# Kernel optimization log

Hardware: AMD Instinct MI355X
Metric: run time of the kernel (lower is better)

The kernel has to match this reference:

```python
import jax, jax.numpy as jnp
import numpy as np

NUM_ACTIVE = 2  # num_active from init


def setup_inputs() -> dict:
    key = jax.random.key(0)
    k1, k2, k3, k4 = jax.random.split(key, 4)
    B, S, D, H, E = 2, 1024, 1024, 4096, 8
    x = jax.random.normal(k1, (B, S, D), jnp.float32)
    # router initialized to zeros in the torch module, but we use small random
    # weights so routing is non-degenerate for the correctness baseline
    router_w = jax.random.normal(k2, (D, E), jnp.float32) * 0.02
    router_b = jnp.zeros((E,), jnp.float32)
    w12 = jax.random.normal(k3, (E, D, 2 * H), jnp.float32) * (1.0 / np.sqrt(D))
    w3 = jax.random.normal(k4, (E, H, D), jnp.float32) * (1.0 / np.sqrt(H))
    return {"x": x, "router_w": router_w, "router_b": router_b, "w12": w12, "w3": w3}


def reference(x, router_w, router_b, w12, w3):
    E = router_w.shape[-1]
    # router (eval mode: no jitter noise)
    logits = x @ router_w + router_b                      # [B,S,E]
    scores = jax.nn.sigmoid(logits)
    top_s, top_i = jax.lax.top_k(scores, NUM_ACTIVE)      # [B,S,k]
    rw = top_s / (jnp.sum(top_s, axis=-1, keepdims=True) + 1e-6)
    # per-token combine weight for each expert: sum of routed slot weights
    cw = jnp.sum(jax.nn.one_hot(top_i, E, dtype=x.dtype) * rw[..., None], axis=-2)  # [B,S,E]
    # dense all-expert SwiGLU (same math as masked loop in the original)
    x12 = jnp.einsum('bsd,edh->ebsh', x, w12)             # [E,B,S,2H]
    x1, x2 = jnp.split(x12, 2, axis=-1)
    h = jax.nn.silu(x1) * x2                              # [E,B,S,H]
    out = jnp.einsum('ebsh,ehd,bse->bsd', h, w3, cw)      # [B,S,D]
    aux_loss = 0.01 * jnp.mean(logits ** 2)
    return out, aux_loss
```

## Files before the change

### kernel.cpp

```cpp
#include <hip/hip_runtime.h>
#include <hip/hip_bf16.h>

#define TOK 2048
#define DIM 1024
#define HID 4096
#define NE  8

typedef short bf16x8 __attribute__((ext_vector_type(8)));
typedef float f32x4 __attribute__((ext_vector_type(4)));
typedef unsigned short ushort_t;
typedef unsigned int uint_t;

#define SWZB(n) (((((n) >> 2) ^ ((n) >> 4)) & 3) << 4)

__device__ __forceinline__ ushort_t f2bf(float f) {
  uint_t b = __float_as_uint(f);
  uint_t r = (b + 0x7FFFu + ((b >> 16) & 1u)) >> 16;
  return (ushort_t)r;
}
__device__ __forceinline__ float bf2f(ushort_t u) {
  return __uint_as_float(((uint_t)u) << 16);
}
__device__ __forceinline__ uint_t pk2bf(float a, float b) {
  uint_t r;
  asm("v_cvt_pk_bf16_f32 %0, %1, %2" : "=v"(r) : "v"(a), "v"(b));
  return r;
}

__global__ void router_kernel(const float* __restrict__ x,
                              const float* __restrict__ rw,
                              const float* __restrict__ rb,
                              float* __restrict__ tok_ss,
                              int* __restrict__ top_e,
                              float* __restrict__ top_w,
                              ushort_t* __restrict__ xb) {
  const int t = blockIdx.x;
  const int lane = threadIdx.x;
  float acc[NE];
#pragma unroll
  for (int e = 0; e < NE; ++e) acc[e] = 0.f;
  const float4* x4 = (const float4*)(x + (size_t)t * DIM);
  uint2* xb2 = (uint2*)(xb + (size_t)t * DIM);
#pragma unroll
  for (int j = 0; j < 4; ++j) {
    int i = j * 64 + lane;
    float4 v = x4[i];
    uint2 u;
    u.x = pk2bf(v.x, v.y);
    u.y = pk2bf(v.z, v.w);
    xb2[i] = u;
    const float* w = rw + (size_t)i * 4 * NE;
    const float* vp = (const float*)&v;
#pragma unroll
    for (int c = 0; c < 4; ++c)
#pragma unroll
      for (int e = 0; e < NE; ++e) acc[e] += vp[c] * w[c * NE + e];
  }
#pragma unroll
  for (int e = 0; e < NE; ++e) {
    float v = acc[e];
#pragma unroll
    for (int off = 32; off > 0; off >>= 1) v += __shfl_down(v, off, 64);
    acc[e] = v;
  }
  if (lane == 0) {
    float sc[NE];
    float ss = 0.f;
#pragma unroll
    for (int e = 0; e < NE; ++e) {
      float lg = acc[e] + rb[e];
      ss += lg * lg;
      sc[e] = 1.f / (1.f + expf(-lg));
    }
    tok_ss[t] = ss;
    int i0 = 0;
#pragma unroll
    for (int e = 1; e < NE; ++e) if (sc[e] > sc[i0]) i0 = e;
    int i1 = (i0 == 0) ? 1 : 0;
#pragma unroll
    for (int e = 0; e < NE; ++e) if (e != i0 && sc[e] > sc[i1]) i1 = e;
    float s0 = sc[i0], s1 = sc[i1];
    float inv = 1.f / (s0 + s1 + 1e-6f);
    top_e[t * 2 + 0] = i0;
    top_e[t * 2 + 1] = i1;
    top_w[t * 2 + 0] = s0 * inv;
    top_w[t * 2 + 1] = s1 * inv;
  }
}

__global__ void scan_assign_kernel(const int* __restrict__ top_e,
                                   const float* __restrict__ top_w,
                                   int* __restrict__ offsets,
                                   int* __restrict__ list_tok,
                                   float* __restrict__ list_w,
                                   int* __restrict__ pair_pos) {
  __shared__ int lcount[NE];
  __shared__ int loff[NE + 1];
  __shared__ int lfill[NE];
  if (threadIdx.x < NE) lcount[threadIdx.x] = 0;
  __syncthreads();
  for (int i = threadIdx.x; i < TOK * 2; i += 256)
    atomicAdd(&lcount[top_e[i]], 1);
  __syncthreads();
  if (threadIdx.x == 0) {
    int o = 0;
    for (int e = 0; e < NE; ++e) { loff[e] = o; lfill[e] = o; o += lcount[e]; }
    loff[NE] = o;
  }
  __syncthreads();
  if (threadIdx.x <= NE) offsets[threadIdx.x] = loff[threadIdx.x];
  for (int i = threadIdx.x; i < TOK * 2; i += 256) {
    int e = top_e[i];
    int idx = atomicAdd(&lfill[e], 1);
    list_tok[idx] = i >> 1;
    list_w[idx] = top_w[i];
    pair_pos[i] = idx;
  }
}

__global__ void aux_kernel(const float* __restrict__ tok_ss, float* __restrict__ out_aux) {
  __shared__ float sm[256];
  float s = 0.f;
  for (int t = threadIdx.x; t < TOK; t += 256) s += tok_ss[t];
  sm[threadIdx.x] = s;
  __syncthreads();
  for (int w = 128; w > 0; w >>= 1) {
    if (threadIdx.x < w) sm[threadIdx.x] += sm[threadIdx.x + w];
    __syncthreads();
  }
  if (threadIdx.x == 0) *out_aux = 0.01f * sm[0] / (float)(TOK * NE);
}

__global__ __launch_bounds__(256)
void gemm1_mfma(const ushort_t* __restrict__ xb,
                const float* __restrict__ w12,
                const int* __restrict__ offsets, const int* __restrict__ list_tok,
                ushort_t* __restrict__ hhi) {
  __shared__ __align__(16) ushort_t Ah[128 * 40];
  __shared__ __align__(16) ushort_t B1[128 * 40];
  __shared__ __align__(16) ushort_t B2[128 * 40];
  __shared__ int stok[128];

  const int e = blockIdx.y >> 4;
  const int rt = blockIdx.y & 15;
  const int rowstart = offsets[e] + rt * 128;
  const int rowend = offsets[e + 1];
  if (rowstart >= rowend) return;
  const int h0 = blockIdx.x * 128;
  const int tid = threadIdx.x;
  const int lane = tid & 63, wid = tid >> 6;
  const int wm = wid >> 1, wn = wid & 1;
  const int lr = lane & 15, kh = lane >> 4;

  if (tid < 128) {
    int r = rowstart + tid;
    stok[tid] = list_tok[r < rowend ? r : rowstart];
  }
  __syncthreads();

  f32x4 acc1[4][4], acc2[4][4];
#pragma unroll
  for (int mi = 0; mi < 4; ++mi)
#pragma unroll
    for (int nj = 0; nj < 4; ++nj) {
      acc1[mi][nj] = (f32x4){0.f, 0.f, 0.f, 0.f};
      acc2[mi][nj] = (f32x4){0.f, 0.f, 0.f, 0.f};
    }

  const int arow0 = tid >> 2, aseg = tid & 3;
  const int arow1 = arow0 + 64;
  const size_t asrc0 = (size_t)stok[arow0] * DIM + aseg * 8;
  const size_t asrc1 = (size_t)stok[arow1] * DIM + aseg * 8;
  const int adst0 = arow0 * 40 + aseg * 8;
  const int adst1 = arow1 * 40 + aseg * 8;

  const int p = tid >> 4, n4 = tid & 15;
  const float* w12e = w12 + (size_t)e * DIM * (2 * HID) + h0 + n4 * 4;
  char* B1c = (char*)B1;
  char* B2c = (char*)B2;

  int boff[4];
#pragma unroll
  for (int nj = 0; nj < 4; ++nj) {
    int n = wn * 64 + nj * 16 + lr;
    boff[nj] = n * 80 + ((kh * 16) ^ SWZB(n));
  }
  int bwoff[4], bwoff2[4];
#pragma unroll
  for (int c = 0; c < 4; ++c) {
    int n = n4 * 4 + c;
    bwoff[c] = n * 80 + ((4 * p) ^ SWZB(n));
    int n2 = 64 + n;
    bwoff2[c] = n2 * 80 + ((4 * p) ^ SWZB(n2));
  }

  uint4 ra0, ra1;
  float4 w1a, w1b, w1c, w1d, w2a, w2b, w2c, w2d;
#define G1_LOAD(K0) do { \
    ra0 = *(const uint4*)&xb[asrc0 + (K0)]; \
    ra1 = *(const uint4*)&xb[asrc1 + (K0)]; \
    const float* r0 = w12e + (size_t)((K0) + 2 * p) * (2 * HID); \
    w1a = *(const float4*)r0; \
    w1b = *(const float4*)(r0 + 2 * HID); \
    w1c = *(const float4*)(r0 + 64); \
    w1d = *(const float4*)(r0 + 2 * HID + 64); \
    w2a = *(const float4*)(r0 + HID); \
    w2b = *(const float4*)(r0 + HID + 2 * HID); \
    w2c = *(const float4*)(r0 + HID + 64); \
    w2d = *(const float4*)(r0 + HID + 2 * HID + 64); \
  } while (0)

  G1_LOAD(0);
#pragma unroll 1
  for (int k0 = 0; k0 < DIM; k0 += 32) {
    *(uint4*)&Ah[adst0] = ra0;
    *(uint4*)&Ah[adst1] = ra1;
    {
      const float* p1a = (const float*)&w1a;
      const float* p1b = (const float*)&w1b;
      const float* p1c = (const float*)&w1c;
      const float* p1d = (const float*)&w1d;
      const float* p2a = (const float*)&w2a;
      const float* p2b = (const float*)&w2b;
      const float* p2c = (const float*)&w2c;
      const float* p2d = (const float*)&w2d;
#pragma unroll
      for (int c = 0; c < 4; ++c) {
        *(uint_t*)(B1c + bwoff[c])  = pk2bf(p1a[c], p1b[c]);
        *(uint_t*)(B2c + bwoff[c])  = pk2bf(p2a[c], p2b[c]);
        *(uint_t*)(B1c + bwoff2[c]) = pk2bf(p1c[c], p1d[c]);
        *(uint_t*)(B2c + bwoff2[c]) = pk2bf(p2c[c], p2d[c]);
      }
    }
    __syncthreads();
    if (k0 + 32 < DIM) G1_LOAD(k0 + 32);

    bf16x8 af[4], b1f[4], b2f[4];
#pragma unroll
    for (int mi = 0; mi < 4; ++mi)
      af[mi] = *(bf16x8*)&Ah[(wm * 64 + mi * 16 + lr) * 40 + kh * 8];
#pragma unroll
    for (int nj = 0; nj < 4; ++nj) {
      b1f[nj] = *(bf16x8*)(B1c + boff[nj]);
      b2f[nj] = *(bf16x8*)(B2c + boff[nj]);
    }
#pragma unroll
    for (int mi = 0; mi < 4; ++mi)
#pragma unroll
      for (int nj = 0; nj < 4; ++nj) {
        acc1[mi][nj] = __builtin_amdgcn_mfma_f32_16x16x32_bf16(af[mi], b1f[nj], acc1[mi][nj], 0, 0, 0);
        acc2[mi][nj] = __builtin_amdgcn_mfma_f32_16x16x32_bf16(af[mi], b2f[nj], acc2[mi][nj], 0, 0, 0);
      }
    __syncthreads();
  }
#undef G1_LOAD

#pragma unroll
  for (int mi = 0; mi < 4; ++mi)
#pragma unroll
    for (int nj = 0; nj < 4; ++nj)
#pragma unroll
      for (int r = 0; r < 4; ++r) {
        int row_t = wm * 64 + mi * 16 + kh * 4 + r;
        int gr = rowstart + row_t;
        if (gr < rowend) {
          int col = h0 + wn * 64 + nj * 16 + lr;
          float v1 = acc1[mi][nj][r], v2 = acc2[mi][nj][r];
          float hv = (v1 / (1.f + expf(-v1))) * v2;
          hhi[(size_t)gr * HID + col] = f2bf(hv);
        }
      }
}

__global__ __launch_bounds__(256)
void gemm2_mfma(const ushort_t* __restrict__ hhi,
                const float* __restrict__ w3,
                const int* __restrict__ offsets, const float* __restrict__ list_w,
                ushort_t* __restrict__ pairout) {
  __shared__ __align__(16) ushort_t As0[64 * 40];
  __shared__ __align__(16) ushort_t As1[64 * 40];
  __shared__ __align__(16) ushort_t Bs0[64 * 40];
  __shared__ __align__(16) ushort_t Bs1[64 * 40];

  const int e = blockIdx.y >> 4;
  const int rt = blockIdx.y & 15;
  const int rowstart = offsets[e] + rt * 64;
  const int rowend = offsets[e + 1];
  if (rowstart >= rowend) return;
  const int d0 = blockIdx.x * 64;
  const int tid = threadIdx.x;
  const int lane = tid & 63, wid = tid >> 6;
  const int wm = wid >> 1, wn = wid & 1;
  const int lr = lane & 15, kh = lane >> 4;

  f32x4 acc[2][2];
#pragma unroll
  for (int mi = 0; mi < 2; ++mi)
#pragma unroll
    for (int nj = 0; nj < 2; ++nj) acc[mi][nj] = (f32x4){0.f, 0.f, 0.f, 0.f};

  const int arow = tid >> 2, aseg = tid & 3;
  int gr = rowstart + arow; if (gr >= rowend) gr = rowstart;
  const size_t asrc = (size_t)gr * HID + aseg * 8;
  const int adst = arow * 40 + aseg * 8;

  const int p = tid >> 4, n4 = tid & 15;
  const float* w3e = w3 + (size_t)e * HID * DIM + d0 + n4 * 4;
  char* Bs0c = (char*)Bs0;
  char* Bs1c = (char*)Bs1;

  int boff[2];
#pragma unroll
  for (int nj = 0; nj < 2; ++nj) {
    int n = wn * 32 + nj * 16 + lr;
    boff[nj] = n * 80 + ((kh * 16) ^ SWZB(n));
  }
  int bwoff[4];
#pragma unroll
  for (int c = 0; c < 4; ++c) {
    int n = n4 * 4 + c;
    bwoff[c] = n * 80 + ((4 * p) ^ SWZB(n));
  }

  uint4 ra0, ra1;
  float4 rb00, rb01, rb10, rb11;
#define G2_LOAD(K0) do { \
    ra0 = *(const uint4*)&hhi[asrc + (K0)]; \
    ra1 = *(const uint4*)&hhi[asrc + (K0) + 32]; \
    const float* r0 = w3e + (size_t)((K0) + 2 * p) * DIM; \
    rb00 = *(const float4*)r0; \
    rb01 = *(const float4*)(r0 + DIM); \
    const float* r1 = w3e + (size_t)((K0) + 32 + 2 * p) * DIM; \
    rb10 = *(const float4*)r1; \
    rb11 = *(const float4*)(r1 + DIM); \
  } while (0)

  const int NT = HID / 64;
  G2_LOAD(0);
#pragma unroll 1
  for (int k0 = 0; k0 < HID; k0 += 64) {
    *(uint4*)&As0[adst] = ra0;
    *(uint4*)&As1[adst] = ra1;
    {
      const float* pv0 = (const float*)&rb00;
      const float* pv1 = (const float*)&rb01;
      const float* pw0 = (const float*)&rb10;
      const float* pw1 = (const float*)&rb11;
#pragma unroll
      for (int c = 0; c < 4; ++c) {
        *(uint_t*)(Bs0c + bwoff[c]) = pk2bf(pv0[c], pv1[c]);
        *(uint_t*)(Bs1c + bwoff[c]) = pk2bf(pw0[c], pw1[c]);
      }
    }
    __syncthreads();
    if (k0 + 64 < HID) G2_LOAD(k0 + 64);

    {
      bf16x8 af[2], bf[2];
#pragma unroll
      for (int mi = 0; mi < 2; ++mi)
        af[mi] = *(bf16x8*)&As0[(wm * 32 + mi * 16 + lr) * 40 + kh * 8];
#pragma unroll
      for (int nj = 0; nj < 2; ++nj)
        bf[nj] = *(bf16x8*)(Bs0c + boff[nj]);
#pragma unroll
      for (int mi = 0; mi < 2; ++mi)
#pragma unroll
        for (int nj = 0; nj < 2; ++nj)
          acc[mi][nj] = __builtin_amdgcn_mfma_f32_16x16x32_bf16(af[mi], bf[nj], acc[mi][nj], 0, 0, 0);
    }
    {
      bf16x8 af[2], bf[2];
#pragma unroll
      for (int mi = 0; mi < 2; ++mi)
        af[mi] = *(bf16x8*)&As1[(wm * 32 + mi * 16 + lr) * 40 + kh * 8];
#pragma unroll
      for (int nj = 0; nj < 2; ++nj)
        bf[nj] = *(bf16x8*)(Bs1c + boff[nj]);
#pragma unroll
      for (int mi = 0; mi < 2; ++mi)
#pragma unroll
        for (int nj = 0; nj < 2; ++nj)
          acc[mi][nj] = __builtin_amdgcn_mfma_f32_16x16x32_bf16(af[mi], bf[nj], acc[mi][nj], 0, 0, 0);
    }
    __syncthreads();
  }
#undef G2_LOAD

#pragma unroll
  for (int mi = 0; mi < 2; ++mi)
#pragma unroll
    for (int nj = 0; nj < 2; ++nj)
#pragma unroll
      for (int r = 0; r < 4; ++r) {
        int grr = rowstart + wm * 32 + mi * 16 + kh * 4 + r;
        if (grr < rowend) {
          int col = d0 + wn * 32 + nj * 16 + lr;
          pairout[(size_t)grr * DIM + col] = f2bf(acc[mi][nj][r] * list_w[grr]);
        }
      }
}

__global__ void combine_bf(const ushort_t* __restrict__ pairout,
                           const int* __restrict__ pair_pos,
                           float* __restrict__ out) {
  int i = blockIdx.x * 256 + threadIdx.x;
  int t = i >> 8;
  int dv = i & 255;
  int p0 = pair_pos[2 * t], p1 = pair_pos[2 * t + 1];
  ushort4 a = *(const ushort4*)&pairout[(size_t)p0 * DIM + dv * 4];
  ushort4 b = *(const ushort4*)&pairout[(size_t)p1 * DIM + dv * 4];
  float4 o;
  o.x = bf2f(a.x) + bf2f(b.x);
  o.y = bf2f(a.y) + bf2f(b.y);
  o.z = bf2f(a.z) + bf2f(b.z);
  o.w = bf2f(a.w) + bf2f(b.w);
  ((float4*)out)[i] = o;
}

extern "C" void kernel_launch(void* const* d_in, const int* in_sizes, int n_in,
                              void* d_out, int out_size, void* d_ws, size_t ws_size,
                              hipStream_t stream) {
  const float* x   = (const float*)d_in[0];
  const float* rw  = (const float*)d_in[1];
  const float* rb  = (const float*)d_in[2];
  const float* w12 = (const float*)d_in[3];
  const float* w3  = (const float*)d_in[4];
  float* out = (float*)d_out;

  char* ws = (char*)d_ws;
  size_t off = 0;
  auto alloc = [&](size_t bytes) {
    void* p = ws + off;
    off = (off + bytes + 255) & ~255ULL;
    return p;
  };
  int*   offsets  = (int*)alloc((NE + 1) * 4);
  float* tok_ss   = (float*)alloc(TOK * 4);
  int*   top_e    = (int*)alloc(TOK * 2 * 4);
  float* top_w    = (float*)alloc(TOK * 2 * 4);
  int*   list_tok = (int*)alloc(TOK * 2 * 4);
  float* list_w   = (float*)alloc(TOK * 2 * 4);
  int*   pair_pos = (int*)alloc(TOK * 2 * 4);

  ushort_t* xb      = (ushort_t*)alloc((size_t)TOK * DIM * 2);
  ushort_t* hhi     = (ushort_t*)alloc((size_t)TOK * 2 * HID * 2);
  ushort_t* pairoutb= (ushort_t*)alloc((size_t)TOK * 2 * DIM * 2);

  hipLaunchKernelGGL(router_kernel, dim3(TOK), dim3(64), 0, stream,
                     x, rw, rb, tok_ss, top_e, top_w, xb);
  hipLaunchKernelGGL(scan_assign_kernel, dim3(1), dim3(256), 0, stream,
                     top_e, top_w, offsets, list_tok, list_w, pair_pos);
  hipLaunchKernelGGL(aux_kernel, dim3(1), dim3(256), 0, stream,
                     tok_ss, out + (size_t)TOK * DIM);

  hipLaunchKernelGGL(gemm1_mfma, dim3(HID / 128, NE * 16), dim3(256), 0, stream,
                     xb, w12, offsets, list_tok, hhi);
  hipLaunchKernelGGL(gemm2_mfma, dim3(DIM / 64, NE * 16), dim3(256), 0, stream,
                     hhi, w3, offsets, list_w, pairoutb);
  hipLaunchKernelGGL(combine_bf, dim3(TOK * DIM / 4 / 256), dim3(256), 0, stream,
                     pairoutb, pair_pos, out);
}
```

Before: 356.4 us.

## Fuse combine into gemm2 via atomics; narrow gemm1 tile with 64-wide K steps

Removes the separate combine kernel and the bf16 pairout buffer. gemm2 now scatters its weighted results straight into the fp32 output with atomicAdd, after a memset of the output. gemm1's N tile is halved to 64 columns, which doubles the grid, and each iteration now handles a K step of 64 in two 32-wide halves, so there are half as many barriers. The atomics add contention, the per-token sum order becomes nondeterministic, and gemm1 now re-reads the activations across twice as many column blocks.

```diff
diff --git a/kernel.cpp b/kernel.cpp
--- a/kernel.cpp
+++ b/kernel.cpp
@@ -92,8 +92,7 @@
                                    const float* __restrict__ top_w,
                                    int* __restrict__ offsets,
                                    int* __restrict__ list_tok,
-                                   float* __restrict__ list_w,
-                                   int* __restrict__ pair_pos) {
+                                   float* __restrict__ list_w) {
   __shared__ int lcount[NE];
   __shared__ int loff[NE + 1];
   __shared__ int lfill[NE];
@@ -114,7 +113,6 @@
     int idx = atomicAdd(&lfill[e], 1);
     list_tok[idx] = i >> 1;
     list_w[idx] = top_w[i];
-    pair_pos[i] = idx;
   }
 }
 
@@ -136,9 +134,12 @@
                 const float* __restrict__ w12,
                 const int* __restrict__ offsets, const int* __restrict__ list_tok,
                 ushort_t* __restrict__ hhi) {
-  __shared__ __align__(16) ushort_t Ah[128 * 40];
-  __shared__ __align__(16) ushort_t B1[128 * 40];
-  __shared__ __align__(16) ushort_t B2[128 * 40];
+  __shared__ __align__(16) ushort_t Ah0[128 * 40];
+  __shared__ __align__(16) ushort_t Ah1[128 * 40];
+  __shared__ __align__(16) ushort_t B1h0[64 * 40];
+  __shared__ __align__(16) ushort_t B1h1[64 * 40];
+  __shared__ __align__(16) ushort_t B2h0[64 * 40];
+  __shared__ __align__(16) ushort_t B2h1[64 * 40];
   __shared__ int stok[128];
 
   const int e = blockIdx.y >> 4;
@@ -146,7 +147,7 @@
   const int rowstart = offsets[e] + rt * 128;
   const int rowend = offsets[e + 1];
   if (rowstart >= rowend) return;
-  const int h0 = blockIdx.x * 128;
+  const int h0 = blockIdx.x * 64;
   const int tid = threadIdx.x;
   const int lane = tid & 63, wid = tid >> 6;
   const int wm = wid >> 1, wn = wid & 1;
@@ -158,11 +159,11 @@
   }
   __syncthreads();
 
-  f32x4 acc1[4][4], acc2[4][4];
+  f32x4 acc1[4][2], acc2[4][2];
 #pragma unroll
   for (int mi = 0; mi < 4; ++mi)
 #pragma unroll
-    for (int nj = 0; nj < 4; ++nj) {
+    for (int nj = 0; nj < 2; ++nj) {
       acc1[mi][nj] = (f32x4){0.f, 0.f, 0.f, 0.f};
       acc2[mi][nj] = (f32x4){0.f, 0.f, 0.f, 0.f};
     }
@@ -176,81 +177,106 @@
 
   const int p = tid >> 4, n4 = tid & 15;
   const float* w12e = w12 + (size_t)e * DIM * (2 * HID) + h0 + n4 * 4;
-  char* B1c = (char*)B1;
-  char* B2c = (char*)B2;
-
-  int boff[4];
-#pragma unroll
-  for (int nj = 0; nj < 4; ++nj) {
-    int n = wn * 64 + nj * 16 + lr;
+  char* B1c0 = (char*)B1h0;
+  char* B1c1 = (char*)B1h1;
+  char* B2c0 = (char*)B2h0;
+  char* B2c1 = (char*)B2h1;
+
+  int boff[2];
+#pragma unroll
+  for (int nj = 0; nj < 2; ++nj) {
+    int n = wn * 32 + nj * 16 + lr;
     boff[nj] = n * 80 + ((kh * 16) ^ SWZB(n));
   }
-  int bwoff[4], bwoff2[4];
+  int bwoff[4];
 #pragma unroll
   for (int c = 0; c < 4; ++c) {
     int n = n4 * 4 + c;
     bwoff[c] = n * 80 + ((4 * p) ^ SWZB(n));
-    int n2 = 64 + n;
-    bwoff2[c] = n2 * 80 + ((4 * p) ^ SWZB(n2));
-  }
-
-  uint4 ra0, ra1;
-  float4 w1a, w1b, w1c, w1d, w2a, w2b, w2c, w2d;
+  }
+
+  uint4 ra00, ra10, ra01, ra11;
+  float4 w1a0, w1b0, w2a0, w2b0, w1a1, w1b1, w2a1, w2b1;
 #define G1_LOAD(K0) do { \
-    ra0 = *(const uint4*)&xb[asrc0 + (K0)]; \
-    ra1 = *(const uint4*)&xb[asrc1 + (K0)]; \
+    ra00 = *(const uint4*)&xb[asrc0 + (K0)]; \
+    ra10 = *(const uint4*)&xb[asrc1 + (K0)]; \
+    ra01 = *(const uint4*)&xb[asrc0 + (K0) + 32]; \
+    ra11 = *(const uint4*)&xb[asrc1 + (K0) + 32]; \
     const float* r0 = w12e + (size_t)((K0) + 2 * p) * (2 * HID); \
-    w1a = *(const float4*)r0; \
-    w1b = *(const float4*)(r0 + 2 * HID); \
-    w1c = *(const float4*)(r0 + 64); \
-    w1d = *(const float4*)(r0 + 2 * HID + 64); \
-    w2a = *(const float4*)(r0 + HID); \
-    w2b = *(const float4*)(r0 + HID + 2 * HID); \
-    w2c = *(const float4*)(r0 + HID + 64); \
-    w2d = *(const float4*)(r0 + HID + 2 * HID + 64); \
+    w1a0 = *(const float4*)r0; \
+    w1b0 = *(const float4*)(r0 + 2 * HID); \
+    w2a0 = *(const float4*)(r0 + HID); \
+    w2b0 = *(const float4*)(r0 + HID + 2 * HID); \
+    const float* r1 = w12e + (size_t)((K0) + 32 + 2 * p) * (2 * HID); \
+    w1a1 = *(const float4*)r1; \
+    w1b1 = *(const float4*)(r1 + 2 * HID); \
+    w2a1 = *(const float4*)(r1 + HID); \
+    w2b1 = *(const float4*)(r1 + HID + 2 * HID); \
   } while (0)
 
   G1_LOAD(0);
 #pragma unroll 1
-  for (int k0 = 0; k0 < DIM; k0 += 32) {
-    *(uint4*)&Ah[adst0] = ra0;
-    *(uint4*)&Ah[adst1] = ra1;
-    {
-      const float* p1a = (const float*)&w1a;
-      const float* p1b = (const float*)&w1b;
-      const float* p1c = (const float*)&w1c;
-      const float* p1d = (const float*)&w1d;
-      const float* p2a = (const float*)&w2a;
-      const float* p2b = (const float*)&w2b;
-      const float* p2c = (const float*)&w2c;
-      const float* p2d = (const float*)&w2d;
+  for (int k0 = 0; k0 < DIM; k0 += 64) {
+    *(uint4*)&Ah0[adst0] = ra00;
+    *(uint4*)&Ah0[adst1] = ra10;
+    *(uint4*)&Ah1[adst0] = ra01;
+    *(uint4*)&Ah1[adst1] = ra11;
+    {
+      const float* p1a0 = (const float*)&w1a0;
+      const float* p1b0 = (const float*)&w1b0;
+      const float* p2a0 = (const float*)&w2a0;
+      const float* p2b0 = (const float*)&w2b0;
+      const float* p1a1 = (const float*)&w1a1;
+      const float* p1b1 = (const float*)&w1b1;
+      const float* p2a1 = (const float*)&w2a1;
+      const float* p2b1 = (const float*)&w2b1;
 #pragma unroll
       for (int c = 0; c < 4; ++c) {
-        *(uint_t*)(B1c + bwoff[c])  = pk2bf(p1a[c], p1b[c]);
-        *(uint_t*)(B2c + bwoff[c])  = pk2bf(p2a[c], p2b[c]);
-        *(uint_t*)(B1c + bwoff2[c]) = pk2bf(p1c[c], p1d[c]);
-        *(uint_t*)(B2c + bwoff2[c]) = pk2bf(p2c[c], p2d[c]);
+        *(uint_t*)(B1c0 + bwoff[c]) = pk2bf(p1a0[c], p1b0[c]);
+        *(uint_t*)(B2c0 + bwoff[c]) = pk2bf(p2a0[c], p2b0[c]);
+        *(uint_t*)(B1c1 + bwoff[c]) = pk2bf(p1a1[c], p1b1[c]);
+        *(uint_t*)(B2c1 + bwoff[c]) = pk2bf(p2a1[c], p2b1[c]);
       }
     }
     __syncthreads();
-    if (k0 + 32 < DIM) G1_LOAD(k0 + 32);
-
-    bf16x8 af[4], b1f[4], b2f[4];
-#pragma unroll
-    for (int mi = 0; mi < 4; ++mi)
-      af[mi] = *(bf16x8*)&Ah[(wm * 64 + mi * 16 + lr) * 40 + kh * 8];
-#pragma unroll
-    for (int nj = 0; nj < 4; ++nj) {
-      b1f[nj] = *(bf16x8*)(B1c + boff[nj]);
-      b2f[nj] = *(bf16x8*)(B2c + boff[nj]);
-    }
-#pragma unroll
-    for (int mi = 0; mi < 4; ++mi)
-#pragma unroll
-      for (int nj = 0; nj < 4; ++nj) {
-        acc1[mi][nj] = __builtin_amdgcn_mfma_f32_16x16x32_bf16(af[mi], b1f[nj], acc1[mi][nj], 0, 0, 0);
-        acc2[mi][nj] = __builtin_amdgcn_mfma_f32_16x16x32_bf16(af[mi], b2f[nj], acc2[mi][nj], 0, 0, 0);
-      }
+    if (k0 + 64 < DIM) G1_LOAD(k0 + 64);
+
+    {
+      bf16x8 af[4], b1f[2], b2f[2];
+#pragma unroll
+      for (int mi = 0; mi < 4; ++mi)
+        af[mi] = *(bf16x8*)&Ah0[(wm * 64 + mi * 16 + lr) * 40 + kh * 8];
+#pragma unroll
+      for (int nj = 0; nj < 2; ++nj) {
+        b1f[nj] = *(bf16x8*)(B1c0 + boff[nj]);
+        b2f[nj] = *(bf16x8*)(B2c0 + boff[nj]);
+      }
+#pragma unroll
+      for (int mi = 0; mi < 4; ++mi)
+#pragma unroll
+        for (int nj = 0; nj < 2; ++nj) {
+          acc1[mi][nj] = __builtin_amdgcn_mfma_f32_16x16x32_bf16(af[mi], b1f[nj], acc1[mi][nj], 0, 0, 0);
+          acc2[mi][nj] = __builtin_amdgcn_mfma_f32_16x16x32_bf16(af[mi], b2f[nj], acc2[mi][nj], 0, 0, 0);
+        }
+    }
+    {
+      bf16x8 af[4], b1f[2], b2f[2];
+#pragma unroll
+      for (int mi = 0; mi < 4; ++mi)
+        af[mi] = *(bf16x8*)&Ah1[(wm * 64 + mi * 16 + lr) * 40 + kh * 8];
+#pragma unroll
+      for (int nj = 0; nj < 2; ++nj) {
+        b1f[nj] = *(bf16x8*)(B1c1 + boff[nj]);
+        b2f[nj] = *(bf16x8*)(B2c1 + boff[nj]);
+      }
+#pragma unroll
+      for (int mi = 0; mi < 4; ++mi)
+#pragma unroll
+        for (int nj = 0; nj < 2; ++nj) {
+          acc1[mi][nj] = __builtin_amdgcn_mfma_f32_16x16x32_bf16(af[mi], b1f[nj], acc1[mi][nj], 0, 0, 0);
+          acc2[mi][nj] = __builtin_amdgcn_mfma_f32_16x16x32_bf16(af[mi], b2f[nj], acc2[mi][nj], 0, 0, 0);
+        }
+    }
     __syncthreads();
   }
 #undef G1_LOAD
@@ -258,13 +284,13 @@
 #pragma unroll
   for (int mi = 0; mi < 4; ++mi)
 #pragma unroll
-    for (int nj = 0; nj < 4; ++nj)
+    for (int nj = 0; nj < 2; ++nj)
 #pragma unroll
       for (int r = 0; r < 4; ++r) {
         int row_t = wm * 64 + mi * 16 + kh * 4 + r;
         int gr = rowstart + row_t;
         if (gr < rowend) {
-          int col = h0 + wn * 64 + nj * 16 + lr;
+          int col = h0 + wn * 32 + nj * 16 + lr;
           float v1 = acc1[mi][nj][r], v2 = acc2[mi][nj][r];
           float hv = (v1 / (1.f + expf(-v1))) * v2;
           hhi[(size_t)gr * HID + col] = f2bf(hv);
@@ -276,7 +302,8 @@
 void gemm2_mfma(const ushort_t* __restrict__ hhi,
                 const float* __restrict__ w3,
                 const int* __restrict__ offsets, const float* __restrict__ list_w,
-                ushort_t* __restrict__ pairout) {
+                const int* __restrict__ list_tok,
+                float* __restrict__ out) {
   __shared__ __align__(16) ushort_t As0[64 * 40];
   __shared__ __align__(16) ushort_t As1[64 * 40];
   __shared__ __align__(16) ushort_t Bs0[64 * 40];
@@ -335,7 +362,6 @@
     rb11 = *(const float4*)(r1 + DIM); \
   } while (0)
 
-  const int NT = HID / 64;
   G2_LOAD(0);
 #pragma unroll 1
   for (int k0 = 0; k0 < HID; k0 += 64) {
@@ -396,26 +422,10 @@
         int grr = rowstart + wm * 32 + mi * 16 + kh * 4 + r;
         if (grr < rowend) {
           int col = d0 + wn * 32 + nj * 16 + lr;
-          pairout[(size_t)grr * DIM + col] = f2bf(acc[mi][nj][r] * list_w[grr]);
+          int tok = list_tok[grr];
+          atomicAdd(&out[(size_t)tok * DIM + col], acc[mi][nj][r] * list_w[grr]);
         }
       }
-}
-
-__global__ void combine_bf(const ushort_t* __restrict__ pairout,
-                           const int* __restrict__ pair_pos,
-                           float* __restrict__ out) {
-  int i = blockIdx.x * 256 + threadIdx.x;
-  int t = i >> 8;
-  int dv = i & 255;
-  int p0 = pair_pos[2 * t], p1 = pair_pos[2 * t + 1];
-  ushort4 a = *(const ushort4*)&pairout[(size_t)p0 * DIM + dv * 4];
-  ushort4 b = *(const ushort4*)&pairout[(size_t)p1 * DIM + dv * 4];
-  float4 o;
-  o.x = bf2f(a.x) + bf2f(b.x);
-  o.y = bf2f(a.y) + bf2f(b.y);
-  o.z = bf2f(a.z) + bf2f(b.z);
-  o.w = bf2f(a.w) + bf2f(b.w);
-  ((float4*)out)[i] = o;
 }
 
 extern "C" void kernel_launch(void* const* d_in, const int* in_sizes, int n_in,
@@ -441,23 +451,21 @@
   float* top_w    = (float*)alloc(TOK * 2 * 4);
   int*   list_tok = (int*)alloc(TOK * 2 * 4);
   float* list_w   = (float*)alloc(TOK * 2 * 4);
-  int*   pair_pos = (int*)alloc(TOK * 2 * 4);
-
-  ushort_t* xb      = (ushort_t*)alloc((size_t)TOK * DIM * 2);
-  ushort_t* hhi     = (ushort_t*)alloc((size_t)TOK * 2 * HID * 2);
-  ushort_t* pairoutb= (ushort_t*)alloc((size_t)TOK * 2 * DIM * 2);
+
+  ushort_t* xb  = (ushort_t*)alloc((size_t)TOK * DIM * 2);
+  ushort_t* hhi = (ushort_t*)alloc((size_t)TOK * 2 * HID * 2);
+
+  hipMemsetAsync(out, 0, (size_t)TOK * DIM * 4, stream);
 
   hipLaunchKernelGGL(router_kernel, dim3(TOK), dim3(64), 0, stream,
                      x, rw, rb, tok_ss, top_e, top_w, xb);
   hipLaunchKernelGGL(scan_assign_kernel, dim3(1), dim3(256), 0, stream,
-                     top_e, top_w, offsets, list_tok, list_w, pair_pos);
+                     top_e, top_w, offsets, list_tok, list_w);
   hipLaunchKernelGGL(aux_kernel, dim3(1), dim3(256), 0, stream,
                      tok_ss, out + (size_t)TOK * DIM);
 
-  hipLaunchKernelGGL(gemm1_mfma, dim3(HID / 128, NE * 16), dim3(256), 0, stream,
+  hipLaunchKernelGGL(gemm1_mfma, dim3(HID / 64, NE * 16), dim3(256), 0, stream,
                      xb, w12, offsets, list_tok, hhi);
   hipLaunchKernelGGL(gemm2_mfma, dim3(DIM / 64, NE * 16), dim3(256), 0, stream,
-                     hhi, w3, offsets, list_w, pairoutb);
-  hipLaunchKernelGGL(combine_bf, dim3(TOK * DIM / 4 / 256), dim3(256), 0, stream,
-                     pairoutb, pair_pos, out);
-}
+                     hhi, w3, offsets, list_w, list_tok, out);
+}
```

Result: faster. 311.5 us (-12.6%).
